# Performance work log

Hardware: AMD Instinct MI355X
Metric: run time of the kernel (lower is better)

## Reference

```python
import jax, jax.numpy as jnp
import numpy as np
from jax import lax

WS = 8       # window size
NH = 16      # num heads
ATT = 64     # att_dim
CH_SCALE = ((ATT // NH) // 2) ** (-0.5)  # (head_dim // key_channels_reduction)**-0.5


def dwconv3(x, w, b):
    # depthwise 3x3, SAME padding; w: [C,1,3,3]
    y = lax.conv_general_dilated(x, w, (1, 1), 'SAME',
                                 feature_group_count=x.shape[1],
                                 dimension_numbers=('NCHW', 'OIHW', 'NCHW'))
    return y + b[None, :, None, None]


def conv1x1(x, w, b):
    # w: [O, C]
    return jnp.einsum('bchw,oc->bohw', x, w) + b[None, :, None, None]


def bn(x, g, b, m, v, eps=1e-5):
    s = g / jnp.sqrt(v + eps)
    return (x - m[None, :, None, None]) * s[None, :, None, None] + b[None, :, None, None]


def to_win(t, h, ws):
    # [B, h*d, H, W] -> [(B*hh*ww), h, ws*ws, d]
    B, C, H, W = t.shape
    d, hh, ww = C // h, H // ws, W // ws
    t = t.reshape(B, h, d, hh, ws, ww, ws).transpose(0, 3, 5, 1, 4, 6, 2)
    return t.reshape(B * hh * ww, h, ws * ws, d)


def from_win(t, B, h, ws, hh, ww):
    # [(B*hh*ww), h, ws*ws, d] -> [B, h*d, H, W]
    d = t.shape[-1]
    t = t.reshape(B, hh, ww, h, ws, ws, d).transpose(0, 3, 6, 1, 4, 2, 5)
    return t.reshape(B, h * d, hh * ws, ww * ws)


def setup_inputs() -> dict:
    key = jax.random.key(0)
    ks = jax.random.split(key, 16)
    C, ATTD, QKC, HID = 64, 64, 32, 256
    B, H, W = 2, 512, 512
    inp = {
        'x': jax.random.normal(ks[0], (B, C, H, W), jnp.float32),
        'pa_w': jax.random.normal(ks[1], (C, 1, 3, 3), jnp.float32) * 0.1,
        'pa_b': jnp.zeros((C,), jnp.float32),
        'bn1_g': jnp.ones((ATTD,), jnp.float32), 'bn1_b': jnp.zeros((ATTD,), jnp.float32),
        'bn1_m': jnp.zeros((ATTD,), jnp.float32), 'bn1_v': jnp.ones((ATTD,), jnp.float32),
        'q_w': jax.random.normal(ks[2], (QKC, C), jnp.float32) * 0.05,
        'q_b': jnp.zeros((QKC,), jnp.float32),
        'k_w': jax.random.normal(ks[3], (QKC, C), jnp.float32) * 0.05,
        'k_b': jnp.zeros((QKC,), jnp.float32),
        'v_w': jax.random.normal(ks[4], (ATTD, C), jnp.float32) * 0.05,
        'v_b': jnp.zeros((ATTD,), jnp.float32),
        'hp_w': jax.random.normal(ks[5], (ATTD, ATTD), jnp.float32) * 0.05,
        'hp_b': jnp.zeros((ATTD,), jnp.float32),
        'bn2_g': jnp.ones((ATTD,), jnp.float32), 'bn2_b': jnp.zeros((ATTD,), jnp.float32),
        'bn2_m': jnp.zeros((ATTD,), jnp.float32), 'bn2_v': jnp.ones((ATTD,), jnp.float32),
        'fc1_w': jax.random.normal(ks[6], (HID, ATTD), jnp.float32) * 0.05,
        'fc1_b': jnp.zeros((HID,), jnp.float32),
        'dw_w': jax.random.normal(ks[7], (HID, 1, 3, 3), jnp.float32) * 0.1,
        'dw_b': jnp.zeros((HID,), jnp.float32),
        'bn3_g': jnp.ones((HID,), jnp.float32), 'bn3_b': jnp.zeros((HID,), jnp.float32),
        'bn3_m': jnp.zeros((HID,), jnp.float32), 'bn3_v': jnp.ones((HID,), jnp.float32),
        'fc2_w': jax.random.normal(ks[8], (ATTD, HID), jnp.float32) * 0.05,
        'fc2_b': jnp.zeros((ATTD,), jnp.float32),
    }
    return inp


def reference(x, pa_w, pa_b, bn1_g, bn1_b, bn1_m, bn1_v, q_w, q_b, k_w, k_b,
              v_w, v_b, hp_w, hp_b, bn2_g, bn2_b, bn2_m, bn2_v, fc1_w, fc1_b,
              dw_w, dw_b, bn3_g, bn3_b, bn3_m, bn3_v, fc2_w, fc2_b):
    B, C, H, W = x.shape
    # H, W are multiples of WS, so the reflect pad is a no-op.
    # PA positional attention
    x = x * jax.nn.sigmoid(dwconv3(x, pa_w, pa_b))
    shortcut = x  # [:, :, :H, :W] is identity here
    xn = bn(x, bn1_g, bn1_b, bn1_m, bn1_v)
    q = conv1x1(xn, q_w, q_b)
    k = conv1x1(xn, k_w, k_b)
    v = conv1x1(xn, v_w, v_b)
    hh, ww = H // WS, W // WS
    q = to_win(q, NH, WS)   # [Bw, h, n, dk]
    k = to_win(k, NH, WS)   # [Bw, h, n, dk]
    v = to_win(v, NH, WS)   # [Bw, h, n, dv]
    q = jax.nn.softmax(q, axis=-1)
    k = jax.nn.softmax(k, axis=-2)
    ctx = jnp.einsum('whnd,whne->whde', k, v)          # [Bw, h, dk, dv]
    attn = jnp.einsum('whnd,whde->whne', q, ctx)        # [Bw, h, n, dv]
    dots = jnp.swapaxes(jnp.einsum('whnd,whne->whde', q, k), -2, -1) * CH_SCALE
    dc = (jnp.max(dots, axis=(-2, -1), keepdims=True) +
          jnp.mean(dots, axis=(-2, -1), keepdims=True))  # [Bw, h, 1, 1]
    attn = attn * dc
    s1 = from_win(attn, B, NH, WS, hh, ww)              # [B, ATT, H, W]
    s1 = conv1x1(s1, hp_w, hp_b) + shortcut
    # MLP block
    s2 = bn(s1, bn2_g, bn2_b, bn2_m, bn2_v)
    s2 = conv1x1(s2, fc1_w, fc1_b)
    s2 = jax.nn.gelu(s2, approximate=False)
    s2 = bn(dwconv3(s2, dw_w, dw_b), bn3_g, bn3_b, bn3_m, bn3_v)
    s2 = conv1x1(s2, fc2_w, fc2_b)
    return s1 + s2
```

## Files before the change

### kernel.cpp

```cpp
#include <hip/hip_runtime.h>
#include <stdint.h>

#define HH 512
#define WW 512
#define HW 262144
#define CH 64
#define HID 256

typedef __attribute__((ext_vector_type(8))) short short8;
typedef __attribute__((ext_vector_type(4))) float f32x4;
typedef _Float16 f16x2 __attribute__((ext_vector_type(2)));
typedef _Float16 f16x8 __attribute__((ext_vector_type(8)));

#define WS_QKVB 0
#define WS_F1B  128
#define WS_F2B  384
#define WS_DWP  448
#define WS_W1F  1600
#define WS_W2F  9792
#define WS_WQKV 17984
#define WS_WHP  22080

__device__ __forceinline__ float bf2f(uint16_t u) {
    return __uint_as_float(((uint32_t)u) << 16);
}
__device__ __forceinline__ uint16_t f2bf(float f) {
    uint32_t x = __float_as_uint(f);
    uint32_t r = x + 0x7fffu + ((x >> 16) & 1u);
    return (uint16_t)(r >> 16);
}
__device__ __forceinline__ float h2f(uint16_t u) {
    _Float16 h;
    __builtin_memcpy(&h, &u, 2);
    return (float)h;
}
__device__ __forceinline__ uint16_t f2h(float f) {
    _Float16 h = (_Float16)f;
    uint16_t u;
    __builtin_memcpy(&u, &h, 2);
    return u;
}
__device__ __forceinline__ f16x2 u2h2(uint32_t u) {
    f16x2 r;
    __builtin_memcpy(&r, &u, 4);
    return r;
}
__device__ __forceinline__ uint32_t h22u(f16x2 h) {
    uint32_t u;
    __builtin_memcpy(&u, &h, 4);
    return u;
}
__device__ __forceinline__ uint32_t pkrtz_u32(float a, float b) {
    auto v = __builtin_amdgcn_cvt_pkrtz(a, b);
    uint32_t u;
    __builtin_memcpy(&u, &v, 4);
    return u;
}

__device__ __forceinline__ float gelu_f(float v) {
    float v2 = v * v;
    float m  = v * (-1.5957691216f - 0.0713548162726f * v2);
    float e  = __expf(m);
    return v * __builtin_amdgcn_rcpf(1.f + e);
}

__global__ __launch_bounds__(256) void k0_fold(
    const float* __restrict__ q_w, const float* __restrict__ q_b,
    const float* __restrict__ k_w, const float* __restrict__ k_b,
    const float* __restrict__ v_w, const float* __restrict__ v_b,
    const float* __restrict__ bn1_g, const float* __restrict__ bn1_b,
    const float* __restrict__ bn1_m, const float* __restrict__ bn1_v,
    const float* __restrict__ fc1_w, const float* __restrict__ fc1_b,
    const float* __restrict__ bn2_g, const float* __restrict__ bn2_b,
    const float* __restrict__ bn2_m, const float* __restrict__ bn2_v,
    const float* __restrict__ fc2_w, const float* __restrict__ fc2_b,
    const float* __restrict__ hp_w,
    const float* __restrict__ dw_w, const float* __restrict__ dw_b,
    const float* __restrict__ bn3_g, const float* __restrict__ bn3_b,
    const float* __restrict__ bn3_m, const float* __restrict__ bn3_v,
    float* __restrict__ wsw)
{
    __shared__ float s1s[64], t1s[64], s2s[64], t2s[64], s3s[256], t3s[256];
    int tid = threadIdx.x;
    if (tid < 64) {
        float s = bn1_g[tid] * rsqrtf(bn1_v[tid] + 1e-5f);
        s1s[tid] = s; t1s[tid] = bn1_b[tid] - bn1_m[tid] * s;
        float s2 = bn2_g[tid] * rsqrtf(bn2_v[tid] + 1e-5f);
        s2s[tid] = s2; t2s[tid] = bn2_b[tid] - bn2_m[tid] * s2;
    }
    if (tid < 256) {
        float s = bn3_g[tid] * rsqrtf(bn3_v[tid] + 1e-5f);
        s3s[tid] = s;
        t3s[tid] = (dw_b[tid] - bn3_m[tid]) * s + bn3_b[tid];
    }
    __syncthreads();

    float* qkvb = wsw + WS_QKVB;
    float* f1b  = wsw + WS_F1B;
    float* f2b  = wsw + WS_F2B;
    uint16_t* dwph  = (uint16_t*)(wsw + WS_DWP);
    uint16_t* w1f   = (uint16_t*)(wsw + WS_W1F);
    uint16_t* w2f   = (uint16_t*)(wsw + WS_W2F);
    uint16_t* wqkvf = (uint16_t*)(wsw + WS_WQKV);
    uint16_t* whpf  = (uint16_t*)(wsw + WS_WHP);

    if (tid < 128) {
        int o = tid;
        float a;
        if (o < 32) {
            a = q_b[o];
            for (int c = 0; c < 64; c++) a += q_w[o*64+c]*t1s[c];
        } else if (o < 64) {
            a = k_b[o-32];
            for (int c = 0; c < 64; c++) a += k_w[(o-32)*64+c]*t1s[c];
        } else {
            a = v_b[o-64];
            for (int c = 0; c < 64; c++) a += v_w[(o-64)*64+c]*t1s[c];
        }
        qkvb[o] = a;
    }
    if (tid < 256) {
        float a = fc1_b[tid];
        for (int c = 0; c < 64; c++) a += fc1_w[tid*64+c]*t2s[c];
        f1b[tid] = a;
    }
    if (tid < 64) {
        float a = fc2_b[tid];
        for (int c = 0; c < 256; c++) a += fc2_w[tid*256+c]*t3s[c];
        f2b[tid] = a;
    }
    for (int i = tid; i < 8192; i += 256) {
        int nt = i >> 10, rem = i & 1023;
        int k8 = rem >> 7, col = (rem >> 3) & 15, j = rem & 7;
        int o = nt*16 + col, c = k8*8 + j;
        float w;
        if (o < 32)      w = q_w[o*64 + c];
        else if (o < 64) w = k_w[(o-32)*64 + c];
        else             w = v_w[(o-64)*64 + c];
        wqkvf[i] = f2bf(w * s1s[c]);
    }
    for (int i = tid; i < 4096; i += 256) {
        int mt = i >> 10, rem = i & 1023;
        int k8 = rem >> 7, row = (rem >> 3) & 15, j = rem & 7;
        int o = mt*16 + row, c = k8*8 + j;
        whpf[i] = f2bf(hp_w[o*64 + c]);
    }
    for (int i = tid; i < 16384; i += 256) {
        int nt = i >> 10, rem = i & 1023;
        int k8 = rem >> 7, col = (rem >> 3) & 15, j = rem & 7;
        int c = k8*8 + j, o = nt*16 + col;
        w1f[i] = f2bf(fc1_w[o*64 + c] * s2s[c]);
    }
    for (int i = tid; i < 16384; i += 256) {
        int nt = i >> 12, rem = i & 4095;
        int k8 = rem >> 7, col = (rem >> 3) & 15, j = rem & 7;
        int c = k8*8 + j, o = nt*16 + col;
        w2f[i] = f2h(fc2_w[o*256 + c] * s3s[c]);
    }
    for (int i = tid; i < 2304; i += 256) {
        int t = i >> 8, ch = i & 255;
        dwph[i] = f2h(dw_w[ch*9 + t]);
    }
}

__global__ __launch_bounds__(256, 4) void k2_attn(
    const float* __restrict__ x,
    const float* __restrict__ pa_w, const float* __restrict__ pa_b,
    const float* __restrict__ hp_b,
    const float* __restrict__ wsw, uint16_t* __restrict__ s1out)
{
    __shared__ __align__(16) uint16_t regionA[10240];
    __shared__ __align__(16) uint16_t gfrag[4096];
    __shared__ __align__(16) uint16_t afrag[4096];
    uint16_t* xs  = regionA;
    uint16_t* qkv = regionA;

    int tid = threadIdx.x;
    int wave = tid >> 6, l = tid & 63;
    int orig = blockIdx.x;
    int wid = (orig & 7) * 1024 + (orig >> 3);
    int b = wid >> 12;
    int r = wid & 4095;
    int wy = r >> 6, wx = r & 63;
    int y0 = wy*8 - 1;
    int x0g = wx*8 - 4;
    const float* xb = x + (size_t)b * CH * HW;

    #pragma unroll
    for (int k = 0; k < 3; k++) {
        int rr = k*256 + tid;
        if (rr < 640) {
            int c = rr / 10;
            int py = rr - c*10;
            int yy = y0 + py;
            uint16_t* dst = &xs[c*160 + py*16];
            if ((unsigned)yy < 512u) {
                const float* src = &xb[(size_t)c*HW + (size_t)yy*512];
                #pragma unroll
                for (int s = 0; s < 4; s++) {
                    int gx = x0g + s*4;
                    uint16_t tv[4];
                    if (gx >= 0 && gx <= 508) {
                        float4 v = *reinterpret_cast<const float4*>(&src[gx]);
                        tv[0] = f2bf(v.x); tv[1] = f2bf(v.y);
                        tv[2] = f2bf(v.z); tv[3] = f2bf(v.w);
                    } else {
                        #pragma unroll
                        for (int e = 0; e < 4; e++) {
                            int gx2 = gx + e;
                            tv[e] = f2bf(((unsigned)gx2 < 512u) ? src[gx2] : 0.f);
                        }
                    }
                    *reinterpret_cast<uint64_t*>(&dst[s*4]) =
                        *reinterpret_cast<const uint64_t*>(tv);
                }
            } else {
                #pragma unroll
                for (int s = 0; s < 4; s++)
                    *reinterpret_cast<uint64_t*>(&dst[s*4]) = 0ull;
            }
        }
    }
    __syncthreads();

    {
        int c = tid & 63, yh = tid >> 6;
        float pw[9];
        #pragma unroll
        for (int t = 0; t < 9; t++) pw[t] = pa_w[c*9 + t];
        float pb = pa_b[c];
        float va[4][12];
        #pragma unroll
        for (int tr = 0; tr < 4; tr++) {
            const uint16_t* rp = &xs[c*160 + (yh*2 + tr)*16];
            #pragma unroll
            for (int s = 0; s < 6; s++) {
                uint32_t u = *reinterpret_cast<const uint32_t*>(&rp[2 + s*2]);
                va[tr][s*2]   = __uint_as_float(u << 16);
                va[tr][s*2+1] = __uint_as_float(u & 0xffff0000u);
            }
        }
        #pragma unroll
        for (int dy2 = 0; dy2 < 2; dy2++) {
            int y = yh*2 + dy2;
            #pragma unroll
            for (int xx = 0; xx < 8; xx++) {
                float conv = pb;
                #pragma unroll
                for (int dy = 0; dy < 3; dy++)
                    #pragma unroll
                    for (int dx = 0; dx < 3; dx++)
                        conv += va[dy2+dy][xx+1+dx] * pw[dy*3+dx];
                float xc = va[dy2+1][xx+2];
                float gv = xc / (1.f + __expf(-conv));
                int n = y*8 + xx;
                gfrag[(n>>4)*1024 + (c>>3)*128 + (n&15)*8 + (c&7)] = f2bf(gv);
            }
        }
    }
    __syncthreads();

    {
        const uint16_t* wqkv = (const uint16_t*)(wsw + WS_WQKV);
        const float* qkvb = wsw + WS_QKVB;
        f32x4 acc[4][2];
        #pragma unroll
        for (int ntw = 0; ntw < 2; ntw++) {
            float bias = qkvb[(wave*2+ntw)*16 + (l & 15)];
            #pragma unroll
            for (int mt = 0; mt < 4; mt++) acc[mt][ntw] = {bias, bias, bias, bias};
        }
        #pragma unroll
        for (int kb = 0; kb < 2; kb++) {
            short8 a[4];
            #pragma unroll
            for (int mt = 0; mt < 4; mt++)
                a[mt] = *reinterpret_cast<const short8*>(&gfrag[mt*1024 + kb*512 + 8*l]);
            #pragma unroll
            for (int ntw = 0; ntw < 2; ntw++) {
                int nt = wave*2 + ntw;
                short8 bf = *reinterpret_cast<const short8*>(&wqkv[nt*1024 + kb*512 + 8*l]);
                #pragma unroll
                for (int mt = 0; mt < 4; mt++)
                    acc[mt][ntw] = __builtin_amdgcn_mfma_f32_16x16x32_bf16(a[mt], bf, acc[mt][ntw], 0, 0, 0);
            }
        }
        #pragma unroll
        for (int ntw = 0; ntw < 2; ntw++) {
            int o = (wave*2+ntw)*16 + (l & 15);
            #pragma unroll
            for (int mt = 0; mt < 4; mt++) {
                int px0 = mt*16 + (l >> 4)*4;
                uint16_t t[4];
                #pragma unroll
                for (int rr = 0; rr < 4; rr++) t[rr] = f2h(acc[mt][ntw][rr]);
                *reinterpret_cast<uint64_t*>(&qkv[o*68 + px0]) =
                    *reinterpret_cast<const uint64_t*>(t);
            }
        }
    }
    __syncthreads();

    {
        int hd = tid >> 4, l16 = tid & 15;
        float a0[4], a1[4], a2[4], a3[4], a4[4], a5[4], a6[4], a7[4];
        #pragma unroll
        for (int j = 0; j < 4; j++) {
            int px = l16 + 16*j;
            a0[j] = h2f(qkv[(2*hd    )*68 + px]);
            a1[j] = h2f(qkv[(2*hd + 1)*68 + px]);
            a2[j] = h2f(qkv[(32 + 2*hd    )*68 + px]);
            a3[j] = h2f(qkv[(32 + 2*hd + 1)*68 + px]);
            a4[j] = h2f(qkv[(64 + 4*hd    )*68 + px]);
            a5[j] = h2f(qkv[(64 + 4*hd + 1)*68 + px]);
            a6[j] = h2f(qkv[(64 + 4*hd + 2)*68 + px]);
            a7[j] = h2f(qkv[(64 + 4*hd + 3)*68 + px]);
        }
        #pragma unroll
        for (int j = 0; j < 4; j++) {
            float m = fmaxf(a0[j], a1[j]);
            float e0 = __expf(a0[j]-m), e1 = __expf(a1[j]-m);
            float inv = 1.f/(e0+e1);
            a0[j] = e0*inv; a1[j] = e1*inv;
        }
        float m0 = fmaxf(fmaxf(a2[0],a2[1]), fmaxf(a2[2],a2[3]));
        float m1 = fmaxf(fmaxf(a3[0],a3[1]), fmaxf(a3[2],a3[3]));
        #pragma unroll
        for (int s = 1; s < 16; s <<= 1) {
            m0 = fmaxf(m0, __shfl_xor(m0, s, 64));
            m1 = fmaxf(m1, __shfl_xor(m1, s, 64));
        }
        float sum0 = 0.f, sum1 = 0.f;
        #pragma unroll
        for (int j = 0; j < 4; j++) {
            a2[j] = __expf(a2[j]-m0); a3[j] = __expf(a3[j]-m1);
            sum0 += a2[j]; sum1 += a3[j];
        }
        #pragma unroll
        for (int s = 1; s < 16; s <<= 1) {
            sum0 += __shfl_xor(sum0, s, 64);
            sum1 += __shfl_xor(sum1, s, 64);
        }
        float iv0 = 1.f/sum0, iv1 = 1.f/sum1;
        #pragma unroll
        for (int j = 0; j < 4; j++) { a2[j] *= iv0; a3[j] *= iv1; }
        float ctx0[4], ctx1[4];
        #pragma unroll
        for (int e = 0; e < 4; e++) {
            float ve0, ve1, ve2, ve3;
            if (e==0) { ve0=a4[0]; ve1=a4[1]; ve2=a4[2]; ve3=a4[3]; }
            else if (e==1) { ve0=a5[0]; ve1=a5[1]; ve2=a5[2]; ve3=a5[3]; }
            else if (e==2) { ve0=a6[0]; ve1=a6[1]; ve2=a6[2]; ve3=a6[3]; }
            else { ve0=a7[0]; ve1=a7[1]; ve2=a7[2]; ve3=a7[3]; }
            float c0 = a2[0]*ve0 + a2[1]*ve1 + a2[2]*ve2 + a2[3]*ve3;
            float c1 = a3[0]*ve0 + a3[1]*ve1 + a3[2]*ve2 + a3[3]*ve3;
            #pragma unroll
            for (int s = 1; s < 16; s <<= 1) {
                c0 += __shfl_xor(c0, s, 64);
                c1 += __shfl_xor(c1, s, 64);
            }
            ctx0[e] = c0; ctx1[e] = c1;
        }
        float p00=0.f, p01=0.f, p10=0.f, p11=0.f;
        #pragma unroll
        for (int j = 0; j < 4; j++) {
            p00 += a0[j]*a2[j]; p01 += a0[j]*a3[j];
            p10 += a1[j]*a2[j]; p11 += a1[j]*a3[j];
        }
        #pragma unroll
        for (int s = 1; s < 16; s <<= 1) {
            p00 += __shfl_xor(p00, s, 64); p01 += __shfl_xor(p01, s, 64);
            p10 += __shfl_xor(p10, s, 64); p11 += __shfl_xor(p11, s, 64);
        }
        const float CH_SCALE = 0.70710678118654752f;
        p00 *= CH_SCALE; p01 *= CH_SCALE; p10 *= CH_SCALE; p11 *= CH_SCALE;
        float dc = fmaxf(fmaxf(p00,p01), fmaxf(p10,p11)) + 0.25f*(p00+p01+p10+p11);

        #pragma unroll
        for (int j = 0; j < 4; j++) {
            uint16_t t[4];
            #pragma unroll
            for (int e = 0; e < 4; e++)
                t[e] = f2bf((a0[j]*ctx0[e] + a1[j]*ctx1[e]) * dc);
            *reinterpret_cast<uint64_t*>(
                &afrag[j*1024 + (hd>>1)*128 + l16*8 + (hd&1)*4]) =
                *reinterpret_cast<const uint64_t*>(t);
        }
    }
    __syncthreads();

    {
        const uint16_t* whp = (const uint16_t*)(wsw + WS_WHP);
        int nt = wave;
        f32x4 oacc[4];
        #pragma unroll
        for (int mt = 0; mt < 4; mt++) {
            int o0 = mt*16 + (l >> 4)*4;
            float4 hb = *reinterpret_cast<const float4*>(&hp_b[o0]);
            oacc[mt] = {hb.x, hb.y, hb.z, hb.w};
        }
        #pragma unroll
        for (int kb = 0; kb < 2; kb++) {
            short8 bf = *reinterpret_cast<const short8*>(&afrag[nt*1024 + kb*512 + 8*l]);
            #pragma unroll
            for (int mt = 0; mt < 4; mt++) {
                short8 a = *reinterpret_cast<const short8*>(&whp[mt*1024 + kb*512 + 8*l]);
                oacc[mt] = __builtin_amdgcn_mfma_f32_16x16x32_bf16(a, bf, oacc[mt], 0, 0, 0);
            }
        }
        int px = nt*16 + (l & 15);
        int yy = wy*8 + (px >> 3), xx = wx*8 + (px & 7);
        size_t pbase = ((size_t)b * HW + (size_t)yy * 512 + xx) * 64;
        #pragma unroll
        for (int mt = 0; mt < 4; mt++) {
            int o0 = mt*16 + (l >> 4)*4;
            uint64_t gg = *reinterpret_cast<const uint64_t*>(
                &gfrag[(px>>4)*1024 + (o0>>3)*128 + (px&15)*8 + (o0&7)]);
            uint16_t t[4];
            #pragma unroll
            for (int rr = 0; rr < 4; rr++) {
                float g = bf2f((uint16_t)(gg >> (16*rr)));
                t[rr] = f2bf(oacc[mt][rr] + g);
            }
            *reinterpret_cast<uint64_t*>(&s1out[pbase + o0]) =
                *reinterpret_cast<const uint64_t*>(t);
        }
    }
}

__global__ __launch_bounds__(256, 4) void k3_mlp(
    const uint16_t* __restrict__ s1b, const float* __restrict__ wsw,
    float* __restrict__ out)
{
    __shared__ __align__(16) uint16_t sfrag[12288];
    __shared__ __align__(16) uint16_t hbuf[7200];

    const float* f1b = wsw + WS_F1B;
    const float* f2b = wsw + WS_F2B;
    const uint16_t* dwph = (const uint16_t*)(wsw + WS_DWP);
    const uint16_t* w1f  = (const uint16_t*)(wsw + WS_W1F);
    const uint16_t* w2f  = (const uint16_t*)(wsw + WS_W2F);

    int tid = threadIdx.x;
    int wave = tid >> 6, l = tid & 63;
    int hxl = l & 15, cg = l >> 4;
    int X0 = blockIdx.x * 16, Y0 = blockIdx.y * 8;
    int b = blockIdx.z;

    for (int i = tid; i < 1440; i += 256) {
        int px = i >> 3, g = i & 7;
        int hy = px / 18, hx = px - hy*18;
        int yy = Y0 - 1 + hy, xx = X0 - 1 + hx;
        uint4 q = {0u, 0u, 0u, 0u};
        if ((unsigned)yy < 512u && (unsigned)xx < 512u)
            q = *reinterpret_cast<const uint4*>(
                &s1b[((size_t)b*HW + (size_t)yy*512 + xx)*64 + g*8]);
        *reinterpret_cast<uint4*>(&sfrag[(px>>4)*1024 + g*128 + (px&15)*8]) = q;
    }

    f32x4 acc[2][4];
    #pragma unroll
    for (int nt = 0; nt < 4; nt++) {
        float bias = f2b[nt*16 + (l & 15)];
        acc[0][nt] = {bias, bias, bias, bias};
        acc[1][nt] = acc[0][nt];
    }
    __syncthreads();

    for (int cc = 0; cc < 8; cc++) {
        short8 wA[2][2];
        #pragma unroll
        for (int mtw = 0; mtw < 2; mtw++)
            #pragma unroll
            for (int kb = 0; kb < 2; kb++)
                wA[mtw][kb] = *reinterpret_cast<const short8*>(
                    &w1f[(cc*2 + mtw)*1024 + kb*512 + 8*l]);
        float4 hb0 = *reinterpret_cast<const float4*>(&f1b[cc*32      + cg*4]);
        float4 hb1 = *reinterpret_cast<const float4*>(&f1b[cc*32 + 16 + cg*4]);

        for (int pt = wave; pt < 12; pt += 4) {
            f32x4 h0 = {hb0.x, hb0.y, hb0.z, hb0.w};
            f32x4 h1 = {hb1.x, hb1.y, hb1.z, hb1.w};
            #pragma unroll
            for (int kb = 0; kb < 2; kb++) {
                short8 bf = *reinterpret_cast<const short8*>(&sfrag[pt*1024 + kb*512 + 8*l]);
                h0 = __builtin_amdgcn_mfma_f32_16x16x32_bf16(wA[0][kb], bf, h0, 0, 0, 0);
                h1 = __builtin_amdgcn_mfma_f32_16x16x32_bf16(wA[1][kb], bf, h1, 0, 0, 0);
            }
            int px = pt*16 + hxl;
            if (px < 180) {
                int hy = px / 18, hx = px - hy*18;
                bool img = ((unsigned)(Y0-1+hy) < 512u) && ((unsigned)(X0-1+hx) < 512u);
                uint64_t v0 = 0, v1 = 0;
                if (img) {
                    uint32_t a01 = pkrtz_u32(gelu_f(h0[0]), gelu_f(h0[1]));
                    uint32_t a23 = pkrtz_u32(gelu_f(h0[2]), gelu_f(h0[3]));
                    uint32_t b01 = pkrtz_u32(gelu_f(h1[0]), gelu_f(h1[1]));
                    uint32_t b23 = pkrtz_u32(gelu_f(h1[2]), gelu_f(h1[3]));
                    v0 = (uint64_t)a01 | ((uint64_t)a23 << 32);
                    v1 = (uint64_t)b01 | ((uint64_t)b23 << 32);
                }
                int base = (hy*18 + hx)*40 + cg*4;
                *reinterpret_cast<uint64_t*>(&hbuf[base])      = v0;
                *reinterpret_cast<uint64_t*>(&hbuf[base + 16]) = v1;
            }
        }
        __syncthreads();

        f16x8 bfr[4];
        #pragma unroll
        for (int nt = 0; nt < 4; nt++)
            bfr[nt] = *reinterpret_cast<const f16x8*>(&w2f[nt*4096 + cc*512 + 8*l]);

        uint4 R[4][3];
        #pragma unroll
        for (int tr = 0; tr < 4; tr++)
            #pragma unroll
            for (int dx = 0; dx < 3; dx++)
                R[tr][dx] = *reinterpret_cast<const uint4*>(
                    &hbuf[((wave*2 + tr)*18 + hxl + dx)*40 + cg*8]);

        union { f16x2 h[4]; f16x8 v; } t0, t1;
        f16x2 z = {(_Float16)0.f, (_Float16)0.f};
        #pragma unroll
        for (int g = 0; g < 4; g++) { t0.h[g] = z; t1.h[g] = z; }

        #pragma unroll
        for (int dy = 0; dy < 3; dy++) {
            #pragma unroll
            for (int dx = 0; dx < 3; dx++) {
                uint4 w = *reinterpret_cast<const uint4*>(
                    &dwph[(dy*3+dx)*256 + cc*32 + cg*8]);
                uint4 qa = R[dy][dx];
                uint4 qb = R[dy+1][dx];
                t0.h[0] += u2h2(qa.x) * u2h2(w.x);
                t0.h[1] += u2h2(qa.y) * u2h2(w.y);
                t0.h[2] += u2h2(qa.z) * u2h2(w.z);
                t0.h[3] += u2h2(qa.w) * u2h2(w.w);
                t1.h[0] += u2h2(qb.x) * u2h2(w.x);
                t1.h[1] += u2h2(qb.y) * u2h2(w.y);
                t1.h[2] += u2h2(qb.z) * u2h2(w.z);
                t1.h[3] += u2h2(qb.w) * u2h2(w.w);
            }
        }
        #pragma unroll
        for (int nt = 0; nt < 4; nt++) {
            acc[0][nt] = __builtin_amdgcn_mfma_f32_16x16x32_f16(t0.v, bfr[nt], acc[0][nt], 0, 0, 0);
            acc[1][nt] = __builtin_amdgcn_mfma_f32_16x16x32_f16(t1.v, bfr[nt], acc[1][nt], 0, 0, 0);
        }
        __syncthreads();
    }

    int r0 = cg * 4;
    #pragma unroll
    for (int mi = 0; mi < 2; mi++) {
        int yrow = Y0 + wave*2 + mi;
        size_t srow = ((size_t)b*HW + (size_t)yrow*512 + X0 + r0) * 64;
        #pragma unroll
        for (int nt = 0; nt < 4; nt++) {
            int o = nt*16 + (l & 15);
            size_t oidx = ((size_t)b*CH + o)*HW + (size_t)yrow*512 + X0 + r0;
            float4 ov;
            ov.x = acc[mi][nt][0] + bf2f(s1b[srow + o]);
            ov.y = acc[mi][nt][1] + bf2f(s1b[srow + 64 + o]);
            ov.z = acc[mi][nt][2] + bf2f(s1b[srow + 128 + o]);
            ov.w = acc[mi][nt][3] + bf2f(s1b[srow + 192 + o]);
            *reinterpret_cast<float4*>(out + oidx) = ov;
        }
    }
}

extern "C" void kernel_launch(void* const* d_in, const int* in_sizes, int n_in,
                              void* d_out, int out_size, void* d_ws, size_t ws_size,
                              hipStream_t stream) {
    const float* x     = (const float*)d_in[0];
    const float* pa_w  = (const float*)d_in[1];
    const float* pa_b  = (const float*)d_in[2];
    const float* bn1_g = (const float*)d_in[3];
    const float* bn1_b = (const float*)d_in[4];
    const float* bn1_m = (const float*)d_in[5];
    const float* bn1_v = (const float*)d_in[6];
    const float* q_w   = (const float*)d_in[7];
    const float* q_b   = (const float*)d_in[8];
    const float* k_w   = (const float*)d_in[9];
    const float* k_b   = (const float*)d_in[10];
    const float* v_w   = (const float*)d_in[11];
    const float* v_b   = (const float*)d_in[12];
    const float* hp_w  = (const float*)d_in[13];
    const float* hp_b  = (const float*)d_in[14];
    const float* bn2_g = (const float*)d_in[15];
    const float* bn2_b = (const float*)d_in[16];
    const float* bn2_m = (const float*)d_in[17];
    const float* bn2_v = (const float*)d_in[18];
    const float* fc1_w = (const float*)d_in[19];
    const float* fc1_b = (const float*)d_in[20];
    const float* dw_w  = (const float*)d_in[21];
    const float* dw_b  = (const float*)d_in[22];
    const float* bn3_g = (const float*)d_in[23];
    const float* bn3_b = (const float*)d_in[24];
    const float* bn3_m = (const float*)d_in[25];
    const float* bn3_v = (const float*)d_in[26];
    const float* fc2_w = (const float*)d_in[27];
    const float* fc2_b = (const float*)d_in[28];

    uint16_t* s1b = (uint16_t*)d_ws;
    float*    wsw = (float*)((char*)d_ws + 134217728 + 268435456);

    k0_fold<<<dim3(1), dim3(256), 0, stream>>>(
        q_w, q_b, k_w, k_b, v_w, v_b,
        bn1_g, bn1_b, bn1_m, bn1_v,
        fc1_w, fc1_b, bn2_g, bn2_b, bn2_m, bn2_v,
        fc2_w, fc2_b, hp_w, dw_w, dw_b, bn3_g, bn3_b, bn3_m, bn3_v, wsw);

    k2_attn<<<dim3(8192), dim3(256), 0, stream>>>(
        x, pa_w, pa_b, hp_b, wsw, s1b);

    k3_mlp<<<dim3(32, 64, 2), dim3(256), 0, stream>>>(
        s1b, wsw, (float*)d_out);
}
```

Baseline: 346.3 us.

## Load attention input straight from global into registers, skipping LDS staging

The attention kernel no longer stages the bf16 x tile in shared memory. Each thread now reads its own fp32 rows from global memory with vector loads, which removes a barrier and shrinks the LDS footprint. The qkv fp16 conversion now uses packed round-toward-zero converts instead of per-element casts. The MLP kernel's hidden buffer pixel stride drops from 40 to 36 halfwords to cut LDS size and change the bank mapping. That new stride leaves 16-byte LDS reads only 8-byte aligned, and the direct global loads across channels may coalesce poorly.

```diff
diff --git a/kernel.cpp b/kernel.cpp
--- a/kernel.cpp
+++ b/kernel.cpp
@@ -44,11 +44,6 @@
     f16x2 r;
     __builtin_memcpy(&r, &u, 4);
     return r;
-}
-__device__ __forceinline__ uint32_t h22u(f16x2 h) {
-    uint32_t u;
-    __builtin_memcpy(&u, &h, 4);
-    return u;
 }
 __device__ __forceinline__ uint32_t pkrtz_u32(float a, float b) {
     auto v = __builtin_amdgcn_cvt_pkrtz(a, b);
@@ -169,11 +164,9 @@
     const float* __restrict__ hp_b,
     const float* __restrict__ wsw, uint16_t* __restrict__ s1out)
 {
-    __shared__ __align__(16) uint16_t regionA[10240];
+    __shared__ __align__(16) uint16_t qkv[8704];
     __shared__ __align__(16) uint16_t gfrag[4096];
     __shared__ __align__(16) uint16_t afrag[4096];
-    uint16_t* xs  = regionA;
-    uint16_t* qkv = regionA;
 
     int tid = threadIdx.x;
     int wave = tid >> 6, l = tid & 63;
@@ -183,45 +176,7 @@
     int r = wid & 4095;
     int wy = r >> 6, wx = r & 63;
     int y0 = wy*8 - 1;
-    int x0g = wx*8 - 4;
     const float* xb = x + (size_t)b * CH * HW;
-
-    #pragma unroll
-    for (int k = 0; k < 3; k++) {
-        int rr = k*256 + tid;
-        if (rr < 640) {
-            int c = rr / 10;
-            int py = rr - c*10;
-            int yy = y0 + py;
-            uint16_t* dst = &xs[c*160 + py*16];
-            if ((unsigned)yy < 512u) {
-                const float* src = &xb[(size_t)c*HW + (size_t)yy*512];
-                #pragma unroll
-                for (int s = 0; s < 4; s++) {
-                    int gx = x0g + s*4;
-                    uint16_t tv[4];
-                    if (gx >= 0 && gx <= 508) {
-                        float4 v = *reinterpret_cast<const float4*>(&src[gx]);
-                        tv[0] = f2bf(v.x); tv[1] = f2bf(v.y);
-                        tv[2] = f2bf(v.z); tv[3] = f2bf(v.w);
-                    } else {
-                        #pragma unroll
-                        for (int e = 0; e < 4; e++) {
-                            int gx2 = gx + e;
-                            tv[e] = f2bf(((unsigned)gx2 < 512u) ? src[gx2] : 0.f);
-                        }
-                    }
-                    *reinterpret_cast<uint64_t*>(&dst[s*4]) =
-                        *reinterpret_cast<const uint64_t*>(tv);
-                }
-            } else {
-                #pragma unroll
-                for (int s = 0; s < 4; s++)
-                    *reinterpret_cast<uint64_t*>(&dst[s*4]) = 0ull;
-            }
-        }
-    }
-    __syncthreads();
 
     {
         int c = tid & 63, yh = tid >> 6;
@@ -229,15 +184,27 @@
         #pragma unroll
         for (int t = 0; t < 9; t++) pw[t] = pa_w[c*9 + t];
         float pb = pa_b[c];
+        const float* xc = xb + (size_t)c * HW;
+        int px0 = wx*8 - 2;
+
         float va[4][12];
         #pragma unroll
         for (int tr = 0; tr < 4; tr++) {
-            const uint16_t* rp = &xs[c*160 + (yh*2 + tr)*16];
-            #pragma unroll
-            for (int s = 0; s < 6; s++) {
-                uint32_t u = *reinterpret_cast<const uint32_t*>(&rp[2 + s*2]);
-                va[tr][s*2]   = __uint_as_float(u << 16);
-                va[tr][s*2+1] = __uint_as_float(u & 0xffff0000u);
+            int yy = y0 + yh*2 + tr;
+            if ((unsigned)yy < 512u) {
+                const float* rp = xc + (size_t)yy*512 + px0;
+                float2 s0 = {0.f, 0.f}, s3 = {0.f, 0.f};
+                if (wx > 0)  s0 = *reinterpret_cast<const float2*>(rp);
+                float4 s1v = *reinterpret_cast<const float4*>(rp + 2);
+                float4 s2v = *reinterpret_cast<const float4*>(rp + 6);
+                if (wx < 63) s3 = *reinterpret_cast<const float2*>(rp + 10);
+                va[tr][0]=s0.x;  va[tr][1]=s0.y;
+                va[tr][2]=s1v.x; va[tr][3]=s1v.y; va[tr][4]=s1v.z; va[tr][5]=s1v.w;
+                va[tr][6]=s2v.x; va[tr][7]=s2v.y; va[tr][8]=s2v.z; va[tr][9]=s2v.w;
+                va[tr][10]=s3.x; va[tr][11]=s3.y;
+            } else {
+                #pragma unroll
+                for (int s = 0; s < 12; s++) va[tr][s] = 0.f;
             }
         }
         #pragma unroll
@@ -251,8 +218,8 @@
                     #pragma unroll
                     for (int dx = 0; dx < 3; dx++)
                         conv += va[dy2+dy][xx+1+dx] * pw[dy*3+dx];
-                float xc = va[dy2+1][xx+2];
-                float gv = xc / (1.f + __expf(-conv));
+                float xcv = va[dy2+1][xx+2];
+                float gv = xcv / (1.f + __expf(-conv));
                 int n = y*8 + xx;
                 gfrag[(n>>4)*1024 + (c>>3)*128 + (n&15)*8 + (c&7)] = f2bf(gv);
             }
@@ -291,11 +258,10 @@
             #pragma unroll
             for (int mt = 0; mt < 4; mt++) {
                 int px0 = mt*16 + (l >> 4)*4;
-                uint16_t t[4];
-                #pragma unroll
-                for (int rr = 0; rr < 4; rr++) t[rr] = f2h(acc[mt][ntw][rr]);
+                uint32_t lo = pkrtz_u32(acc[mt][ntw][0], acc[mt][ntw][1]);
+                uint32_t hi = pkrtz_u32(acc[mt][ntw][2], acc[mt][ntw][3]);
                 *reinterpret_cast<uint64_t*>(&qkv[o*68 + px0]) =
-                    *reinterpret_cast<const uint64_t*>(t);
+                    (uint64_t)lo | ((uint64_t)hi << 32);
             }
         }
     }
@@ -433,7 +399,7 @@
     float* __restrict__ out)
 {
     __shared__ __align__(16) uint16_t sfrag[12288];
-    __shared__ __align__(16) uint16_t hbuf[7200];
+    __shared__ __align__(16) uint16_t hbuf[6480];
 
     const float* f1b = wsw + WS_F1B;
     const float* f2b = wsw + WS_F2B;
@@ -500,7 +466,7 @@
                     v0 = (uint64_t)a01 | ((uint64_t)a23 << 32);
                     v1 = (uint64_t)b01 | ((uint64_t)b23 << 32);
                 }
-                int base = (hy*18 + hx)*40 + cg*4;
+                int base = px*36 + cg*4;
                 *reinterpret_cast<uint64_t*>(&hbuf[base])      = v0;
                 *reinterpret_cast<uint64_t*>(&hbuf[base + 16]) = v1;
             }
@@ -518,7 +484,7 @@
             #pragma unroll
             for (int dx = 0; dx < 3; dx++)
                 R[tr][dx] = *reinterpret_cast<const uint4*>(
-                    &hbuf[((wave*2 + tr)*18 + hxl + dx)*40 + cg*8]);
+                    &hbuf[((wave*2 + tr)*18 + hxl + dx)*36 + cg*8]);
 
         union { f16x2 h[4]; f16x8 v; } t0, t1;
         f16x2 z = {(_Float16)0.f, (_Float16)0.f};
```

New measurement: 342.4 us. About the same (-1.1%).
